# Performance work log

Measured on AMD Instinct MI355X. Metric: run time of the kernel, lower is better.

The kernel has to match this reference:

```python
import jax, jax.numpy as jnp
import numpy as np

D = 256   # state.D, per-node vector width
B = 16    # batch
L = 8     # depth layers (hidden), all < t_budget
N = 128   # nodes per depth layer
LAMBDA_ASYNC = 0.08
LAMBDA_TAU = 0.12
BOOST_SCALE = 1.0


def setup_inputs() -> dict:
    key = jax.random.key(0)
    ks = jax.random.split(key, 6)
    X = jax.random.normal(ks[0], (B, D), jnp.float32)
    # per-node weight matrices, scaled so tanh stays in linear-ish regime
    W = jax.random.normal(ks[1], (L, N, D, D), jnp.float32) / np.sqrt(D).astype(np.float32)
    bias = jax.random.normal(ks[2], (L, N, D), jnp.float32) * 0.01
    S = jax.random.normal(ks[3], (L, N, D), jnp.float32) / np.sqrt(D).astype(np.float32)
    rho = jax.random.uniform(ks[4], (L, N), jnp.float32, minval=0.2, maxval=0.6)
    boost = jax.random.normal(ks[5], (L, N), jnp.float32) * 0.01  # residue.decode(node_id)
    return {"X": X, "W": W, "bias": bias, "S": S, "rho": rho, "boost": boost, "t_budget": 15}


def reference(X, W, bias, S, rho, boost, t_budget):
    # Messages routed at depth d are consumed at depth d+1 -> decay = exp(-lambda_async * 1)
    decay = jnp.exp(jnp.float32(-LAMBDA_ASYNC))
    tb = jnp.float32(t_budget)

    def step(carry, layer):
        V_in, has_input = carry            # V_in: (B, D) aggregated inbox, shared under dense routing
        Wl, bl, Sl, rl, gl, depth = layer  # (N,D,D), (N,D), (N,D), (N,), (N,), scalar
        # anytime threshold tau(t) = 0.5 * exp(lambda_tau * (t - t_budget))
        tau = 0.5 * jnp.exp(LAMBDA_TAU * (depth - tb))
        # s_dot.mean(): mean over batch of <V_in, S_n>, per node -> (N,)
        s_dot = jnp.einsum('bd,nd->n', V_in, Sl) / jnp.float32(B)
        rho_active = rl + s_dot + gl * BOOST_SCALE
        fired = (rho_active >= tau) & has_input                      # (N,) thresholded firing
        # V_weighted = apply_W_batch(V_in) + bias, per node
        V_w = jnp.einsum('bd,nde->nbe', V_in, Wl) + bl[:, None, :]   # (N, B, D)
        V_out = jnp.tanh(V_w)                                        # pointwise primitive
        fmask = fired.astype(V_out.dtype)
        cnt = jnp.maximum(fmask.sum(), jnp.float32(1.0))
        # inbox aggregation at next depth: decayed mean over fired contributors
        V_next = decay * jnp.einsum('n,nbe->be', fmask, V_out) / cnt
        return (V_next, fmask.sum() > 0), (V_out, fired)

    depths = jnp.arange(1, L + 1, dtype=jnp.float32)
    (_, _), (V_all, fired_all) = jax.lax.scan(
        step, (X, jnp.array(True)), (W, bias, S, rho, boost, depths))
    # output = mean over fired output-layer (last depth) nodes
    last_V, last_f = V_all[-1], fired_all[-1]
    fm = last_f.astype(last_V.dtype)
    out = jnp.einsum('n,nbe->be', fm, last_V) / jnp.maximum(fm.sum(), jnp.float32(1.0))
    return out
```

## Files before the change

### kernel.cpp

```cpp
#include <hip/hip_runtime.h>
#include <math.h>

#define D 256
#define B 16
#define L 8
#define N 128

static constexpr float LAMBDA_ASYNC = 0.08f;
static constexpr float LAMBDA_TAU   = 0.12f;


#define OFF_META  32768
#define OFF_FIRED 32784
#define OFF_SLAB  33808

__global__ __launch_bounds__(512, 2) void layer_kernel(
    const float* __restrict__ Wl,
    const float* __restrict__ biasl,
    const float* __restrict__ Sl,
    const float* __restrict__ rhol,
    const float* __restrict__ boostl,
    const int*  __restrict__ tb,
    const float* __restrict__ vin_src,
    const float* __restrict__ X,
    const float* __restrict__ meta_prev,
    float* __restrict__ slab,
    float* __restrict__ fired_cur,
    float depth, int is_first)
{
    __shared__ float vin[D * 16];
    __shared__ float red[4 * 64 * 33];
    __shared__ float sh[8];

    const int t    = threadIdx.x;
    const int w    = t >> 6;
    const int lane = t & 63;
    const int n    = blockIdx.x >> 1;
    const int e0   = (blockIdx.x & 1) * 128;

    if (is_first) {
        #pragma unroll
        for (int k = 0; k < 2; ++k) {
            const float4 xv = ((const float4*)X)[t * 2 + k];
            const int idx = (t * 2 + k) * 4;
            const int b   = idx >> 8;
            const int d0  = idx & 255;
            vin[(d0 + 0) * 16 + b] = xv.x;
            vin[(d0 + 1) * 16 + b] = xv.y;
            vin[(d0 + 2) * 16 + b] = xv.z;
            vin[(d0 + 3) * 16 + b] = xv.w;
        }
    } else {
        const float4* s4 = (const float4*)vin_src;
        ((float4*)vin)[t * 2 + 0] = s4[t * 2 + 0];
        ((float4*)vin)[t * 2 + 1] = s4[t * 2 + 1];
    }
    __syncthreads();

    float part = 0.0f;
    if (t < 256) {
        const float4 a0 = *(const float4*)&vin[t * 16 + 0];
        const float4 a1 = *(const float4*)&vin[t * 16 + 4];
        const float4 a2 = *(const float4*)&vin[t * 16 + 8];
        const float4 a3 = *(const float4*)&vin[t * 16 + 12];
        const float cs = a0.x + a0.y + a0.z + a0.w + a1.x + a1.y + a1.z + a1.w
                       + a2.x + a2.y + a2.z + a2.w + a3.x + a3.y + a3.z + a3.w;
        part = cs * Sl[n * D + t];
    }
    #pragma unroll
    for (int o = 32; o > 0; o >>= 1) part += __shfl_down(part, o);
    if (lane == 0) sh[w] = part;
    __syncthreads();

    {
        const bool has_input = is_first ? true : (meta_prev[0] > 0.0f);
        const float sdot = (sh[0] + sh[1] + sh[2] + sh[3]) * (1.0f / 16.0f);
        const float tau  = 0.5f * expf(LAMBDA_TAU * (depth - (float)tb[0]));
        const bool fired = (rhol[n] + sdot + boostl[n] >= tau) && has_input;
        if (e0 == 0 && t == 0) fired_cur[n] = fired ? 1.0f : 0.0f;
        if (!fired) return;
    }

    const float* wp = Wl + (size_t)n * D * D + (e0 + lane * 2);
    const int dbase = w * 32;

    float accA[16], accB[16];
    #pragma unroll
    for (int b = 0; b < 16; ++b) { accA[b] = 0.0f; accB[b] = 0.0f; }

    #pragma unroll
    for (int j = 0; j < 32; j += 4) {
        float2 wv[4];
        #pragma unroll
        for (int i = 0; i < 4; ++i)
            wv[i] = *(const float2*)(wp + (size_t)(dbase + j + i) * 256);
        #pragma unroll
        for (int i = 0; i < 4; ++i) {
            const float* vr = &vin[(dbase + j + i) * 16];
            const float4 v0 = *(const float4*)(vr + 0);
            const float4 v1 = *(const float4*)(vr + 4);
            const float4 v2 = *(const float4*)(vr + 8);
            const float4 v3 = *(const float4*)(vr + 12);
            const float wx = wv[i].x, wy = wv[i].y;
            accA[ 0] = fmaf(wx, v0.x, accA[ 0]); accB[ 0] = fmaf(wy, v0.x, accB[ 0]);
            accA[ 1] = fmaf(wx, v0.y, accA[ 1]); accB[ 1] = fmaf(wy, v0.y, accB[ 1]);
            accA[ 2] = fmaf(wx, v0.z, accA[ 2]); accB[ 2] = fmaf(wy, v0.z, accB[ 2]);
            accA[ 3] = fmaf(wx, v0.w, accA[ 3]); accB[ 3] = fmaf(wy, v0.w, accB[ 3]);
            accA[ 4] = fmaf(wx, v1.x, accA[ 4]); accB[ 4] = fmaf(wy, v1.x, accB[ 4]);
            accA[ 5] = fmaf(wx, v1.y, accA[ 5]); accB[ 5] = fmaf(wy, v1.y, accB[ 5]);
            accA[ 6] = fmaf(wx, v1.z, accA[ 6]); accB[ 6] = fmaf(wy, v1.z, accB[ 6]);
            accA[ 7] = fmaf(wx, v1.w, accA[ 7]); accB[ 7] = fmaf(wy, v1.w, accB[ 7]);
            accA[ 8] = fmaf(wx, v2.x, accA[ 8]); accB[ 8] = fmaf(wy, v2.x, accB[ 8]);
            accA[ 9] = fmaf(wx, v2.y, accA[ 9]); accB[ 9] = fmaf(wy, v2.y, accB[ 9]);
            accA[10] = fmaf(wx, v2.z, accA[10]); accB[10] = fmaf(wy, v2.z, accB[10]);
            accA[11] = fmaf(wx, v2.w, accA[11]); accB[11] = fmaf(wy, v2.w, accB[11]);
            accA[12] = fmaf(wx, v3.x, accA[12]); accB[12] = fmaf(wy, v3.x, accB[12]);
            accA[13] = fmaf(wx, v3.y, accA[13]); accB[13] = fmaf(wy, v3.y, accB[13]);
            accA[14] = fmaf(wx, v3.z, accA[14]); accB[14] = fmaf(wy, v3.z, accB[14]);
            accA[15] = fmaf(wx, v3.w, accA[15]); accB[15] = fmaf(wy, v3.w, accB[15]);
        }
    }

    {
        float* rr = &red[((w & 3) * 64 + lane) * 33];
        if (w >= 4) {
            #pragma unroll
            for (int b = 0; b < 16; ++b) { rr[b] = accA[b]; rr[16 + b] = accB[b]; }
        }
        __syncthreads();
        if (w < 4) {
            #pragma unroll
            for (int b = 0; b < 16; ++b) { rr[b] += accA[b]; rr[16 + b] += accB[b]; }
        }
        __syncthreads();
    }

    {
        const int e_loc = t >> 2;
        const int b0    = (t & 3) * 4;
        const int lane2 = e_loc >> 1;
        const int sub   = e_loc & 1;
        const float bv  = biasl[n * D + e0 + e_loc];
        float* dst = slab + (size_t)n * 4096 + (size_t)(e0 + e_loc) * 16 + b0;
        const int o0 = sub * 16 + b0;
        float4 o4;
        o4.x = tanhf(red[(0*64+lane2)*33 + o0+0] + red[(1*64+lane2)*33 + o0+0]
                   + red[(2*64+lane2)*33 + o0+0] + red[(3*64+lane2)*33 + o0+0] + bv);
        o4.y = tanhf(red[(0*64+lane2)*33 + o0+1] + red[(1*64+lane2)*33 + o0+1]
                   + red[(2*64+lane2)*33 + o0+1] + red[(3*64+lane2)*33 + o0+1] + bv);
        o4.z = tanhf(red[(0*64+lane2)*33 + o0+2] + red[(1*64+lane2)*33 + o0+2]
                   + red[(2*64+lane2)*33 + o0+2] + red[(3*64+lane2)*33 + o0+2] + bv);
        o4.w = tanhf(red[(0*64+lane2)*33 + o0+3] + red[(1*64+lane2)*33 + o0+3]
                   + red[(2*64+lane2)*33 + o0+3] + red[(3*64+lane2)*33 + o0+3] + bv);
        *(float4*)dst = o4;
    }
}

__global__ __launch_bounds__(256) void reduce_mid(
    const float* __restrict__ slab, const float* __restrict__ fired_l,
    float* __restrict__ acct_l, float* __restrict__ meta_l)
{
    __shared__ float part[256];
    __shared__ float shcnt;
    const int t    = threadIdx.x;
    const int cell = blockIdx.x * 64 + (t & 63);
    const int n0   = (t >> 6) * 32;

    float s = 0.0f;
    #pragma unroll 8
    for (int k = 0; k < 32; ++k)
        s = fmaf(fired_l[n0 + k], slab[(size_t)(n0 + k) * 4096 + cell], s);
    part[t] = s;

    if (t < 64) {
        float c = fired_l[t] + fired_l[t + 64];
        #pragma unroll
        for (int o = 32; o > 0; o >>= 1) c += __shfl_down(c, o);
        if (t == 0) shcnt = c;
    }
    __syncthreads();

    if (t < 64) {
        const float cnt   = shcnt;
        const float scale = expf(-LAMBDA_ASYNC) / fmaxf(cnt, 1.0f);
        const float v = part[t] + part[64 + t] + part[128 + t] + part[192 + t];
        acct_l[blockIdx.x * 64 + t] = v * scale;
        if (blockIdx.x == 0 && t == 0) meta_l[0] = cnt;
    }
}

__global__ __launch_bounds__(256) void reduce_final(
    const float* __restrict__ slab, const float* __restrict__ fired_l,
    float* __restrict__ out)
{
    __shared__ float part[256];
    __shared__ float shcnt;
    const int t    = threadIdx.x;
    const int cell = blockIdx.x * 64 + (t & 63);
    const int n0   = (t >> 6) * 32;

    float s = 0.0f;
    #pragma unroll 8
    for (int k = 0; k < 32; ++k)
        s = fmaf(fired_l[n0 + k], slab[(size_t)(n0 + k) * 4096 + cell], s);
    part[t] = s;

    if (t < 64) {
        float c = fired_l[t] + fired_l[t + 64];
        #pragma unroll
        for (int o = 32; o > 0; o >>= 1) c += __shfl_down(c, o);
        if (t == 0) shcnt = c;
    }
    __syncthreads();

    if (t < 64) {
        const float inv = 1.0f / fmaxf(shcnt, 1.0f);
        const int c = blockIdx.x * 64 + t;
        const float v = (part[t] + part[64 + t] + part[128 + t] + part[192 + t]) * inv;
        const int e = c >> 4, b = c & 15;
        out[b * 256 + e] = v;
    }
}

extern "C" void kernel_launch(void* const* d_in, const int* in_sizes, int n_in,
                              void* d_out, int out_size, void* d_ws, size_t ws_size,
                              hipStream_t stream)
{
    const float* X     = (const float*)d_in[0];
    const float* W     = (const float*)d_in[1];
    const float* bias  = (const float*)d_in[2];
    const float* S     = (const float*)d_in[3];
    const float* rho   = (const float*)d_in[4];
    const float* boost = (const float*)d_in[5];
    const int*   tb    = (const int*)d_in[6];
    float* out = (float*)d_out;
    float* ws  = (float*)d_ws;

    float* acct  = ws;
    float* meta  = ws + OFF_META;
    float* fired = ws + OFF_FIRED;
    float* slab  = ws + OFF_SLAB;

    for (int l = 0; l < L; ++l) {
        layer_kernel<<<dim3(256), dim3(512), 0, stream>>>(
            W + (size_t)l * N * D * D,
            bias + (size_t)l * N * D,
            S + (size_t)l * N * D,
            rho + (size_t)l * N,
            boost + (size_t)l * N,
            tb,
            (l == 0) ? (const float*)nullptr : acct + (size_t)(l - 1) * 4096,
            X,
            (l == 0) ? (const float*)nullptr : meta + (l - 1),
            slab,
            fired + (size_t)l * N,
            (float)(l + 1), (l == 0) ? 1 : 0);
        if (l < L - 1) {
            reduce_mid<<<dim3(64), dim3(256), 0, stream>>>(
                slab, fired + (size_t)l * N,
                acct + (size_t)l * 4096, meta + l);
        } else {
            reduce_final<<<dim3(64), dim3(256), 0, stream>>>(
                slab, fired + (size_t)l * N, out);
        }
    }
}
```

Before: 115.9 us.

## Prefetch weights before firing check, precompute column sums, retile layer kernel

The layer kernel now uses 256-thread blocks, with 4 blocks per node each covering 64 output columns. Each block issues its first weight loads before the firing decision and double-buffers the weight rows in registers. The per-batch column sums of the inbox are computed once by the previous reduce kernel (and by a new transpose kernel for X), so the gate no longer needs the inbox staged in shared memory first. Workspace buffers are reused across layers instead of being indexed per layer. In exchange, non-fired blocks may issue wasted weight loads, there is one extra launch, and the accumulator count per thread is lower.

After: 119.3 us. +2.9%, slower.

```diff
diff --git a/kernel.cpp b/kernel.cpp
--- a/kernel.cpp
+++ b/kernel.cpp
@@ -10,11 +10,26 @@
 static constexpr float LAMBDA_TAU   = 0.12f;
 
 
-#define OFF_META  32768
-#define OFF_FIRED 32784
-#define OFF_SLAB  33808
-
-__global__ __launch_bounds__(512, 2) void layer_kernel(
+#define OFF_COLSUM 4096
+#define OFF_META   4352
+#define OFF_FIRED  4368
+#define OFF_SLAB   4496
+
+__global__ __launch_bounds__(256) void transpose_kernel(
+    const float* __restrict__ X, float* __restrict__ xt,
+    float* __restrict__ colsum) {
+    const int d = threadIdx.x;
+    float cs = 0.0f;
+    #pragma unroll
+    for (int b = 0; b < B; ++b) {
+        const float v = X[b * D + d];
+        xt[d * 16 + b] = v;
+        cs += v;
+    }
+    colsum[d] = cs;
+}
+
+__global__ __launch_bounds__(256) void layer_kernel(
     const float* __restrict__ Wl,
     const float* __restrict__ biasl,
     const float* __restrict__ Sl,
@@ -22,56 +37,32 @@
     const float* __restrict__ boostl,
     const int*  __restrict__ tb,
     const float* __restrict__ vin_src,
-    const float* __restrict__ X,
+    const float* __restrict__ colsum,
     const float* __restrict__ meta_prev,
     float* __restrict__ slab,
     float* __restrict__ fired_cur,
     float depth, int is_first)
 {
     __shared__ float vin[D * 16];
-    __shared__ float red[4 * 64 * 33];
-    __shared__ float sh[8];
+    __shared__ float red[4 * 64 * 17];
+    __shared__ float sh[4];
 
     const int t    = threadIdx.x;
     const int w    = t >> 6;
     const int lane = t & 63;
-    const int n    = blockIdx.x >> 1;
-    const int e0   = (blockIdx.x & 1) * 128;
-
-    if (is_first) {
-        #pragma unroll
-        for (int k = 0; k < 2; ++k) {
-            const float4 xv = ((const float4*)X)[t * 2 + k];
-            const int idx = (t * 2 + k) * 4;
-            const int b   = idx >> 8;
-            const int d0  = idx & 255;
-            vin[(d0 + 0) * 16 + b] = xv.x;
-            vin[(d0 + 1) * 16 + b] = xv.y;
-            vin[(d0 + 2) * 16 + b] = xv.z;
-            vin[(d0 + 3) * 16 + b] = xv.w;
-        }
-    } else {
-        const float4* s4 = (const float4*)vin_src;
-        ((float4*)vin)[t * 2 + 0] = s4[t * 2 + 0];
-        ((float4*)vin)[t * 2 + 1] = s4[t * 2 + 1];
-    }
-    __syncthreads();
-
-    float part = 0.0f;
-    if (t < 256) {
-        const float4 a0 = *(const float4*)&vin[t * 16 + 0];
-        const float4 a1 = *(const float4*)&vin[t * 16 + 4];
-        const float4 a2 = *(const float4*)&vin[t * 16 + 8];
-        const float4 a3 = *(const float4*)&vin[t * 16 + 12];
-        const float cs = a0.x + a0.y + a0.z + a0.w + a1.x + a1.y + a1.z + a1.w
-                       + a2.x + a2.y + a2.z + a2.w + a3.x + a3.y + a3.z + a3.w;
-        part = cs * Sl[n * D + t];
-    }
+    const int n    = blockIdx.x >> 2;
+    const int e0   = (blockIdx.x & 3) * 64;
+
+    const float* wp = Wl + ((size_t)n * D + (size_t)(w * 64)) * D + (e0 + lane);
+    float wa[8], wb[8];
+    #pragma unroll
+    for (int i = 0; i < 8; ++i) wa[i] = wp[(size_t)i * D];
+
+    float part = colsum[t] * Sl[n * D + t];
     #pragma unroll
     for (int o = 32; o > 0; o >>= 1) part += __shfl_down(part, o);
     if (lane == 0) sh[w] = part;
     __syncthreads();
-
     {
         const bool has_input = is_first ? true : (meta_prev[0] > 0.0f);
         const float sdot = (sh[0] + sh[1] + sh[2] + sh[3]) * (1.0f / 16.0f);
@@ -81,84 +72,88 @@
         if (!fired) return;
     }
 
-    const float* wp = Wl + (size_t)n * D * D + (e0 + lane * 2);
-    const int dbase = w * 32;
-
-    float accA[16], accB[16];
-    #pragma unroll
-    for (int b = 0; b < 16; ++b) { accA[b] = 0.0f; accB[b] = 0.0f; }
-
-    #pragma unroll
-    for (int j = 0; j < 32; j += 4) {
-        float2 wv[4];
-        #pragma unroll
-        for (int i = 0; i < 4; ++i)
-            wv[i] = *(const float2*)(wp + (size_t)(dbase + j + i) * 256);
-        #pragma unroll
-        for (int i = 0; i < 4; ++i) {
-            const float* vr = &vin[(dbase + j + i) * 16];
+    {
+        const float4* s4 = (const float4*)vin_src;
+        #pragma unroll
+        for (int k = 0; k < 4; ++k)
+            ((float4*)vin)[t * 4 + k] = s4[t * 4 + k];
+    }
+    __syncthreads();
+
+    const int dbase = w * 64;
+    float acc[16];
+    #pragma unroll
+    for (int b = 0; b < 16; ++b) acc[b] = 0.0f;
+
+    #pragma unroll
+    for (int c = 0; c < 8; ++c) {
+        float* cur = (c & 1) ? wb : wa;
+        float* nxt = (c & 1) ? wa : wb;
+        if (c < 7) {
+            #pragma unroll
+            for (int i = 0; i < 8; ++i)
+                nxt[i] = wp[(size_t)((c + 1) * 8 + i) * D];
+        }
+        #pragma unroll
+        for (int i = 0; i < 8; ++i) {
+            const float* vr = &vin[(dbase + c * 8 + i) * 16];
             const float4 v0 = *(const float4*)(vr + 0);
             const float4 v1 = *(const float4*)(vr + 4);
             const float4 v2 = *(const float4*)(vr + 8);
             const float4 v3 = *(const float4*)(vr + 12);
-            const float wx = wv[i].x, wy = wv[i].y;
-            accA[ 0] = fmaf(wx, v0.x, accA[ 0]); accB[ 0] = fmaf(wy, v0.x, accB[ 0]);
-            accA[ 1] = fmaf(wx, v0.y, accA[ 1]); accB[ 1] = fmaf(wy, v0.y, accB[ 1]);
-            accA[ 2] = fmaf(wx, v0.z, accA[ 2]); accB[ 2] = fmaf(wy, v0.z, accB[ 2]);
-            accA[ 3] = fmaf(wx, v0.w, accA[ 3]); accB[ 3] = fmaf(wy, v0.w, accB[ 3]);
-            accA[ 4] = fmaf(wx, v1.x, accA[ 4]); accB[ 4] = fmaf(wy, v1.x, accB[ 4]);
-            accA[ 5] = fmaf(wx, v1.y, accA[ 5]); accB[ 5] = fmaf(wy, v1.y, accB[ 5]);
-            accA[ 6] = fmaf(wx, v1.z, accA[ 6]); accB[ 6] = fmaf(wy, v1.z, accB[ 6]);
-            accA[ 7] = fmaf(wx, v1.w, accA[ 7]); accB[ 7] = fmaf(wy, v1.w, accB[ 7]);
-            accA[ 8] = fmaf(wx, v2.x, accA[ 8]); accB[ 8] = fmaf(wy, v2.x, accB[ 8]);
-            accA[ 9] = fmaf(wx, v2.y, accA[ 9]); accB[ 9] = fmaf(wy, v2.y, accB[ 9]);
-            accA[10] = fmaf(wx, v2.z, accA[10]); accB[10] = fmaf(wy, v2.z, accB[10]);
-            accA[11] = fmaf(wx, v2.w, accA[11]); accB[11] = fmaf(wy, v2.w, accB[11]);
-            accA[12] = fmaf(wx, v3.x, accA[12]); accB[12] = fmaf(wy, v3.x, accB[12]);
-            accA[13] = fmaf(wx, v3.y, accA[13]); accB[13] = fmaf(wy, v3.y, accB[13]);
-            accA[14] = fmaf(wx, v3.z, accA[14]); accB[14] = fmaf(wy, v3.z, accB[14]);
-            accA[15] = fmaf(wx, v3.w, accA[15]); accB[15] = fmaf(wy, v3.w, accB[15]);
-        }
-    }
-
-    {
-        float* rr = &red[((w & 3) * 64 + lane) * 33];
-        if (w >= 4) {
-            #pragma unroll
-            for (int b = 0; b < 16; ++b) { rr[b] = accA[b]; rr[16 + b] = accB[b]; }
-        }
-        __syncthreads();
-        if (w < 4) {
-            #pragma unroll
-            for (int b = 0; b < 16; ++b) { rr[b] += accA[b]; rr[16 + b] += accB[b]; }
-        }
-        __syncthreads();
-    }
+            const float wj = cur[i];
+            acc[ 0] = fmaf(wj, v0.x, acc[ 0]);
+            acc[ 1] = fmaf(wj, v0.y, acc[ 1]);
+            acc[ 2] = fmaf(wj, v0.z, acc[ 2]);
+            acc[ 3] = fmaf(wj, v0.w, acc[ 3]);
+            acc[ 4] = fmaf(wj, v1.x, acc[ 4]);
+            acc[ 5] = fmaf(wj, v1.y, acc[ 5]);
+            acc[ 6] = fmaf(wj, v1.z, acc[ 6]);
+            acc[ 7] = fmaf(wj, v1.w, acc[ 7]);
+            acc[ 8] = fmaf(wj, v2.x, acc[ 8]);
+            acc[ 9] = fmaf(wj, v2.y, acc[ 9]);
+            acc[10] = fmaf(wj, v2.z, acc[10]);
+            acc[11] = fmaf(wj, v2.w, acc[11]);
+            acc[12] = fmaf(wj, v3.x, acc[12]);
+            acc[13] = fmaf(wj, v3.y, acc[13]);
+            acc[14] = fmaf(wj, v3.z, acc[14]);
+            acc[15] = fmaf(wj, v3.w, acc[15]);
+        }
+    }
+
+    {
+        float* rr = &red[(w * 64 + lane) * 17];
+        #pragma unroll
+        for (int b = 0; b < 16; ++b) rr[b] = acc[b];
+    }
+    __syncthreads();
 
     {
         const int e_loc = t >> 2;
         const int b0    = (t & 3) * 4;
-        const int lane2 = e_loc >> 1;
-        const int sub   = e_loc & 1;
         const float bv  = biasl[n * D + e0 + e_loc];
-        float* dst = slab + (size_t)n * 4096 + (size_t)(e0 + e_loc) * 16 + b0;
-        const int o0 = sub * 16 + b0;
         float4 o4;
-        o4.x = tanhf(red[(0*64+lane2)*33 + o0+0] + red[(1*64+lane2)*33 + o0+0]
-                   + red[(2*64+lane2)*33 + o0+0] + red[(3*64+lane2)*33 + o0+0] + bv);
-        o4.y = tanhf(red[(0*64+lane2)*33 + o0+1] + red[(1*64+lane2)*33 + o0+1]
-                   + red[(2*64+lane2)*33 + o0+1] + red[(3*64+lane2)*33 + o0+1] + bv);
-        o4.z = tanhf(red[(0*64+lane2)*33 + o0+2] + red[(1*64+lane2)*33 + o0+2]
-                   + red[(2*64+lane2)*33 + o0+2] + red[(3*64+lane2)*33 + o0+2] + bv);
-        o4.w = tanhf(red[(0*64+lane2)*33 + o0+3] + red[(1*64+lane2)*33 + o0+3]
-                   + red[(2*64+lane2)*33 + o0+3] + red[(3*64+lane2)*33 + o0+3] + bv);
-        *(float4*)dst = o4;
+        float s[4];
+        #pragma unroll
+        for (int q = 0; q < 4; ++q) {
+            const int b = b0 + q;
+            s[q] = red[(0 * 64 + e_loc) * 17 + b]
+                 + red[(1 * 64 + e_loc) * 17 + b]
+                 + red[(2 * 64 + e_loc) * 17 + b]
+                 + red[(3 * 64 + e_loc) * 17 + b];
+        }
+        o4.x = tanhf(s[0] + bv);
+        o4.y = tanhf(s[1] + bv);
+        o4.z = tanhf(s[2] + bv);
+        o4.w = tanhf(s[3] + bv);
+        *(float4*)(slab + (size_t)n * 4096 + (size_t)(e0 + e_loc) * 16 + b0) = o4;
     }
 }
 
 __global__ __launch_bounds__(256) void reduce_mid(
     const float* __restrict__ slab, const float* __restrict__ fired_l,
-    float* __restrict__ acct_l, float* __restrict__ meta_l)
+    float* __restrict__ acct, float* __restrict__ colsum,
+    float* __restrict__ meta)
 {
     __shared__ float part[256];
     __shared__ float shcnt;
@@ -183,9 +178,15 @@
     if (t < 64) {
         const float cnt   = shcnt;
         const float scale = expf(-LAMBDA_ASYNC) / fmaxf(cnt, 1.0f);
-        const float v = part[t] + part[64 + t] + part[128 + t] + part[192 + t];
-        acct_l[blockIdx.x * 64 + t] = v * scale;
-        if (blockIdx.x == 0 && t == 0) meta_l[0] = cnt;
+        float v = (part[t] + part[64 + t] + part[128 + t] + part[192 + t]) * scale;
+        acct[blockIdx.x * 64 + t] = v;
+        float cs = v;
+        cs += __shfl_down(cs, 8);
+        cs += __shfl_down(cs, 4);
+        cs += __shfl_down(cs, 2);
+        cs += __shfl_down(cs, 1);
+        if ((t & 15) == 0) colsum[(blockIdx.x * 64 + t) >> 4] = cs;
+        if (blockIdx.x == 0 && t == 0) meta[0] = cnt;
     }
 }
 
@@ -236,32 +237,34 @@
     float* out = (float*)d_out;
     float* ws  = (float*)d_ws;
 
-    float* acct  = ws;
-    float* meta  = ws + OFF_META;
-    float* fired = ws + OFF_FIRED;
-    float* slab  = ws + OFF_SLAB;
+    float* acct   = ws;
+    float* colsum = ws + OFF_COLSUM;
+    float* meta   = ws + OFF_META;
+    float* fired  = ws + OFF_FIRED;
+    float* slab   = ws + OFF_SLAB;
+
+    transpose_kernel<<<dim3(1), dim3(256), 0, stream>>>(X, acct, colsum);
 
     for (int l = 0; l < L; ++l) {
-        layer_kernel<<<dim3(256), dim3(512), 0, stream>>>(
+        layer_kernel<<<dim3(512), dim3(256), 0, stream>>>(
             W + (size_t)l * N * D * D,
             bias + (size_t)l * N * D,
             S + (size_t)l * N * D,
             rho + (size_t)l * N,
             boost + (size_t)l * N,
             tb,
-            (l == 0) ? (const float*)nullptr : acct + (size_t)(l - 1) * 4096,
-            X,
-            (l == 0) ? (const float*)nullptr : meta + (l - 1),
+            acct,
+            colsum,
+            (l == 0) ? (const float*)nullptr : meta,
             slab,
-            fired + (size_t)l * N,
+            fired,
             (float)(l + 1), (l == 0) ? 1 : 0);
         if (l < L - 1) {
             reduce_mid<<<dim3(64), dim3(256), 0, stream>>>(
-                slab, fired + (size_t)l * N,
-                acct + (size_t)l * 4096, meta + l);
+                slab, fired, acct, colsum, meta);
         } else {
             reduce_final<<<dim3(64), dim3(256), 0, stream>>>(
-                slab, fired + (size_t)l * N, out);
-        }
-    }
-}
+                slab, fired, out);
+        }
+    }
+}
```

## Precompute inbox column sums and move bias+tanh into reduce kernel

Applied to the files above, without the earlier changes.

The reduce kernel now also writes per-feature column sums of the next inbox. The layer kernel uses them for the firing test, so it no longer stages and sums the inbox before deciding. Non-fired blocks now exit before loading the 16KB inbox into shared memory. Bias add and tanh move from the layer kernel into the reduce kernel, which applies them only for fired nodes and skips unfired slab reads. The occupancy hint of 2 blocks per CU is dropped from launch_bounds, which may change register allocation.

Measured after the change: 255.5 us. 120% more time.

```diff
diff --git a/kernel.cpp b/kernel.cpp
--- a/kernel.cpp
+++ b/kernel.cpp
@@ -10,19 +10,20 @@
 static constexpr float LAMBDA_TAU   = 0.12f;
 
 
-#define OFF_META  32768
-#define OFF_FIRED 32784
-#define OFF_SLAB  33808
-
-__global__ __launch_bounds__(512, 2) void layer_kernel(
+#define OFF_COLSUM 4096
+#define OFF_META   4352
+#define OFF_FIRED  4368
+#define OFF_SLAB   4496
+
+__global__ __launch_bounds__(512) void layer_kernel(
     const float* __restrict__ Wl,
-    const float* __restrict__ biasl,
     const float* __restrict__ Sl,
     const float* __restrict__ rhol,
     const float* __restrict__ boostl,
     const int*  __restrict__ tb,
     const float* __restrict__ vin_src,
     const float* __restrict__ X,
+    const float* __restrict__ colsum,
     const float* __restrict__ meta_prev,
     float* __restrict__ slab,
     float* __restrict__ fired_cur,
@@ -36,36 +37,36 @@
     const int w    = t >> 6;
     const int lane = t & 63;
     const int n    = blockIdx.x >> 1;
-    const int e0   = (blockIdx.x & 1) * 128;
-
+    const int h    = blockIdx.x & 1;
+    const int e0   = h * 128;
+
+    float part = 0.0f;
     if (is_first) {
-        #pragma unroll
-        for (int k = 0; k < 2; ++k) {
-            const float4 xv = ((const float4*)X)[t * 2 + k];
-            const int idx = (t * 2 + k) * 4;
-            const int b   = idx >> 8;
-            const int d0  = idx & 255;
-            vin[(d0 + 0) * 16 + b] = xv.x;
-            vin[(d0 + 1) * 16 + b] = xv.y;
-            vin[(d0 + 2) * 16 + b] = xv.z;
-            vin[(d0 + 3) * 16 + b] = xv.w;
+        if (t < 256) {
+            #pragma unroll
+            for (int k = 0; k < 2; ++k) {
+                const float4 xv = ((const float4*)X)[t * 2 + k];
+                const int idx = (t * 2 + k) * 4;
+                const int b   = idx >> 8;
+                const int d0  = idx & 255;
+                vin[(d0 + 0) * 16 + b] = xv.x;
+                vin[(d0 + 1) * 16 + b] = xv.y;
+                vin[(d0 + 2) * 16 + b] = xv.z;
+                vin[(d0 + 3) * 16 + b] = xv.w;
+            }
+        }
+        __syncthreads();
+        if (t < 256) {
+            const float4 a0 = *(const float4*)&vin[t * 16 + 0];
+            const float4 a1 = *(const float4*)&vin[t * 16 + 4];
+            const float4 a2 = *(const float4*)&vin[t * 16 + 8];
+            const float4 a3 = *(const float4*)&vin[t * 16 + 12];
+            const float cs = a0.x + a0.y + a0.z + a0.w + a1.x + a1.y + a1.z + a1.w
+                           + a2.x + a2.y + a2.z + a2.w + a3.x + a3.y + a3.z + a3.w;
+            part = cs * Sl[n * D + t];
         }
     } else {
-        const float4* s4 = (const float4*)vin_src;
-        ((float4*)vin)[t * 2 + 0] = s4[t * 2 + 0];
-        ((float4*)vin)[t * 2 + 1] = s4[t * 2 + 1];
-    }
-    __syncthreads();
-
-    float part = 0.0f;
-    if (t < 256) {
-        const float4 a0 = *(const float4*)&vin[t * 16 + 0];
-        const float4 a1 = *(const float4*)&vin[t * 16 + 4];
-        const float4 a2 = *(const float4*)&vin[t * 16 + 8];
-        const float4 a3 = *(const float4*)&vin[t * 16 + 12];
-        const float cs = a0.x + a0.y + a0.z + a0.w + a1.x + a1.y + a1.z + a1.w
-                       + a2.x + a2.y + a2.z + a2.w + a3.x + a3.y + a3.z + a3.w;
-        part = cs * Sl[n * D + t];
+        if (t < 256) part = colsum[t] * Sl[n * D + t];
     }
     #pragma unroll
     for (int o = 32; o > 0; o >>= 1) part += __shfl_down(part, o);
@@ -77,8 +78,15 @@
         const float sdot = (sh[0] + sh[1] + sh[2] + sh[3]) * (1.0f / 16.0f);
         const float tau  = 0.5f * expf(LAMBDA_TAU * (depth - (float)tb[0]));
         const bool fired = (rhol[n] + sdot + boostl[n] >= tau) && has_input;
-        if (e0 == 0 && t == 0) fired_cur[n] = fired ? 1.0f : 0.0f;
+        if (h == 0 && t == 0) fired_cur[n] = fired ? 1.0f : 0.0f;
         if (!fired) return;
+    }
+
+    if (!is_first) {
+        const float4* s4 = (const float4*)vin_src;
+        ((float4*)vin)[t * 2 + 0] = s4[t * 2 + 0];
+        ((float4*)vin)[t * 2 + 1] = s4[t * 2 + 1];
+        __syncthreads();
     }
 
     const float* wp = Wl + (size_t)n * D * D + (e0 + lane * 2);
@@ -140,36 +148,41 @@
         const int b0    = (t & 3) * 4;
         const int lane2 = e_loc >> 1;
         const int sub   = e_loc & 1;
-        const float bv  = biasl[n * D + e0 + e_loc];
-        float* dst = slab + (size_t)n * 4096 + (size_t)(e0 + e_loc) * 16 + b0;
-        const int o0 = sub * 16 + b0;
+        const int o0    = sub * 16 + b0;
         float4 o4;
-        o4.x = tanhf(red[(0*64+lane2)*33 + o0+0] + red[(1*64+lane2)*33 + o0+0]
-                   + red[(2*64+lane2)*33 + o0+0] + red[(3*64+lane2)*33 + o0+0] + bv);
-        o4.y = tanhf(red[(0*64+lane2)*33 + o0+1] + red[(1*64+lane2)*33 + o0+1]
-                   + red[(2*64+lane2)*33 + o0+1] + red[(3*64+lane2)*33 + o0+1] + bv);
-        o4.z = tanhf(red[(0*64+lane2)*33 + o0+2] + red[(1*64+lane2)*33 + o0+2]
-                   + red[(2*64+lane2)*33 + o0+2] + red[(3*64+lane2)*33 + o0+2] + bv);
-        o4.w = tanhf(red[(0*64+lane2)*33 + o0+3] + red[(1*64+lane2)*33 + o0+3]
-                   + red[(2*64+lane2)*33 + o0+3] + red[(3*64+lane2)*33 + o0+3] + bv);
-        *(float4*)dst = o4;
+        o4.x = red[(0*64+lane2)*33 + o0+0] + red[(1*64+lane2)*33 + o0+0]
+             + red[(2*64+lane2)*33 + o0+0] + red[(3*64+lane2)*33 + o0+0];
+        o4.y = red[(0*64+lane2)*33 + o0+1] + red[(1*64+lane2)*33 + o0+1]
+             + red[(2*64+lane2)*33 + o0+1] + red[(3*64+lane2)*33 + o0+1];
+        o4.z = red[(0*64+lane2)*33 + o0+2] + red[(1*64+lane2)*33 + o0+2]
+             + red[(2*64+lane2)*33 + o0+2] + red[(3*64+lane2)*33 + o0+2];
+        o4.w = red[(0*64+lane2)*33 + o0+3] + red[(1*64+lane2)*33 + o0+3]
+             + red[(2*64+lane2)*33 + o0+3] + red[(3*64+lane2)*33 + o0+3];
+        *(float4*)(slab + (size_t)n * 4096 + (size_t)(e0 + e_loc) * 16 + b0) = o4;
     }
 }
 
-__global__ __launch_bounds__(256) void reduce_mid(
-    const float* __restrict__ slab, const float* __restrict__ fired_l,
-    float* __restrict__ acct_l, float* __restrict__ meta_l)
+template<bool IS_FINAL>
+__global__ __launch_bounds__(256) void reduce_kernel(
+    const float* __restrict__ slab, const float* __restrict__ biasl,
+    const float* __restrict__ fired_l,
+    float* __restrict__ acct, float* __restrict__ colsum,
+    float* __restrict__ meta, float* __restrict__ out)
 {
     __shared__ float part[256];
     __shared__ float shcnt;
     const int t    = threadIdx.x;
     const int cell = blockIdx.x * 64 + (t & 63);
     const int n0   = (t >> 6) * 32;
+    const int e    = cell >> 4;
 
     float s = 0.0f;
-    #pragma unroll 8
-    for (int k = 0; k < 32; ++k)
-        s = fmaf(fired_l[n0 + k], slab[(size_t)(n0 + k) * 4096 + cell], s);
+    for (int k = 0; k < 32; ++k) {
+        const int n = n0 + k;
+        const float f = fired_l[n];
+        if (f > 0.0f)
+            s += tanhf(slab[(size_t)n * 4096 + cell] + biasl[n * D + e]);
+    }
     part[t] = s;
 
     if (t < 64) {
@@ -181,44 +194,23 @@
     __syncthreads();
 
     if (t < 64) {
-        const float cnt   = shcnt;
-        const float scale = expf(-LAMBDA_ASYNC) / fmaxf(cnt, 1.0f);
-        const float v = part[t] + part[64 + t] + part[128 + t] + part[192 + t];
-        acct_l[blockIdx.x * 64 + t] = v * scale;
-        if (blockIdx.x == 0 && t == 0) meta_l[0] = cnt;
-    }
-}
-
-__global__ __launch_bounds__(256) void reduce_final(
-    const float* __restrict__ slab, const float* __restrict__ fired_l,
-    float* __restrict__ out)
-{
-    __shared__ float part[256];
-    __shared__ float shcnt;
-    const int t    = threadIdx.x;
-    const int cell = blockIdx.x * 64 + (t & 63);
-    const int n0   = (t >> 6) * 32;
-
-    float s = 0.0f;
-    #pragma unroll 8
-    for (int k = 0; k < 32; ++k)
-        s = fmaf(fired_l[n0 + k], slab[(size_t)(n0 + k) * 4096 + cell], s);
-    part[t] = s;
-
-    if (t < 64) {
-        float c = fired_l[t] + fired_l[t + 64];
-        #pragma unroll
-        for (int o = 32; o > 0; o >>= 1) c += __shfl_down(c, o);
-        if (t == 0) shcnt = c;
-    }
-    __syncthreads();
-
-    if (t < 64) {
-        const float inv = 1.0f / fmaxf(shcnt, 1.0f);
+        const float cnt = shcnt;
         const int c = blockIdx.x * 64 + t;
-        const float v = (part[t] + part[64 + t] + part[128 + t] + part[192 + t]) * inv;
-        const int e = c >> 4, b = c & 15;
-        out[b * 256 + e] = v;
+        const float tot = part[t] + part[64 + t] + part[128 + t] + part[192 + t];
+        if (IS_FINAL) {
+            out[(c & 15) * 256 + (c >> 4)] = tot / fmaxf(cnt, 1.0f);
+        } else {
+            const float scale = expf(-LAMBDA_ASYNC) / fmaxf(cnt, 1.0f);
+            const float v = tot * scale;
+            acct[c] = v;
+            float cs = v;
+            cs += __shfl_down(cs, 8);
+            cs += __shfl_down(cs, 4);
+            cs += __shfl_down(cs, 2);
+            cs += __shfl_down(cs, 1);
+            if ((t & 15) == 0) colsum[c >> 4] = cs;
+            if (blockIdx.x == 0 && t == 0) meta[0] = cnt;
+        }
     }
 }
 
@@ -236,32 +228,31 @@
     float* out = (float*)d_out;
     float* ws  = (float*)d_ws;
 
-    float* acct  = ws;
-    float* meta  = ws + OFF_META;
-    float* fired = ws + OFF_FIRED;
-    float* slab  = ws + OFF_SLAB;
+    float* acct   = ws;
+    float* colsum = ws + OFF_COLSUM;
+    float* meta   = ws + OFF_META;
+    float* fired  = ws + OFF_FIRED;
+    float* slab   = ws + OFF_SLAB;
 
     for (int l = 0; l < L; ++l) {
         layer_kernel<<<dim3(256), dim3(512), 0, stream>>>(
             W + (size_t)l * N * D * D,
-            bias + (size_t)l * N * D,
             S + (size_t)l * N * D,
             rho + (size_t)l * N,
             boost + (size_t)l * N,
             tb,
-            (l == 0) ? (const float*)nullptr : acct + (size_t)(l - 1) * 4096,
-            X,
-            (l == 0) ? (const float*)nullptr : meta + (l - 1),
-            slab,
-            fired + (size_t)l * N,
+            acct, X, colsum,
+            (l == 0) ? (const float*)nullptr : meta,
+            slab, fired,
             (float)(l + 1), (l == 0) ? 1 : 0);
         if (l < L - 1) {
-            reduce_mid<<<dim3(64), dim3(256), 0, stream>>>(
-                slab, fired + (size_t)l * N,
-                acct + (size_t)l * 4096, meta + l);
+            reduce_kernel<false><<<dim3(64), dim3(256), 0, stream>>>(
+                slab, bias + (size_t)l * N * D, fired,
+                acct, colsum, meta, out);
         } else {
-            reduce_final<<<dim3(64), dim3(256), 0, stream>>>(
-                slab, fired + (size_t)l * N, out);
+            reduce_kernel<true><<<dim3(64), dim3(256), 0, stream>>>(
+                slab, bias + (size_t)l * N * D, fired,
+                acct, colsum, meta, out);
         }
     }
 }
```
